# Optimization experiments

Hardware: AMD Instinct MI355X
Metric: run time of the kernel (lower is better)

The kernel has to match this reference:

```python
import jax, jax.numpy as jnp
import numpy as np

K = 16  # kNN neighbors (global k in the original source)
# channel progression of the 6 DynamicEdgeConv layers
DIMS = [3, 32, 128, 256, 64, 32, 16]


def _knn_idx(x, k):
    # x: [B, N, D] -> indices of k nearest neighbors (incl. self), [B, N, k]
    sq = jnp.sum(x * x, axis=-1)                                   # [B, N]
    d = sq[:, :, None] + sq[:, None, :] - 2.0 * jnp.einsum('bnd,bmd->bnm', x, x)
    _, idx = jax.lax.top_k(-d, k)                                  # smallest distances
    return idx


def _edge_conv(x, W1, b1, W2, b2, k):
    # DynamicEdgeConv with mean aggregation: message = MLP([x_i, x_j - x_i])
    idx = _knn_idx(x, k)                                           # [B, N, k]
    xj = jax.vmap(lambda xb, ib: xb[ib])(x, idx)                   # [B, N, k, D]
    xi = jnp.broadcast_to(x[:, :, None, :], xj.shape)
    e = jnp.concatenate([xi, xj - xi], axis=-1)                    # [B, N, k, 2D]
    h = jax.nn.relu(e @ W1 + b1)
    h = jax.nn.relu(h @ W2 + b2)
    return jnp.mean(h, axis=2)                                     # [B, N, d_out]


def setup_inputs() -> dict:
    key = jax.random.key(0)
    ks = jax.random.split(key, 32)
    inp = {'x': jax.random.normal(ks[0], (8, 2048, 3), dtype=jnp.float32)}
    for l in range(6):
        din, dout = DIMS[l], DIMS[l + 1]
        s1 = 1.0 / np.sqrt(2 * din)
        s2 = 1.0 / np.sqrt(2 * dout)
        inp[f'W1_{l}'] = jax.random.normal(ks[1 + 4 * l], (2 * din, 2 * dout), dtype=jnp.float32) * s1
        inp[f'b1_{l}'] = jnp.zeros((2 * dout,), dtype=jnp.float32)
        inp[f'W2_{l}'] = jax.random.normal(ks[2 + 4 * l], (2 * dout, dout), dtype=jnp.float32) * s2
        inp[f'b2_{l}'] = jnp.zeros((dout,), dtype=jnp.float32)
    inp['Wf'] = jax.random.normal(ks[30], (16, 2), dtype=jnp.float32) * 0.25
    inp['bf'] = jnp.zeros((2,), dtype=jnp.float32)
    return inp


def reference(x, W1_0, b1_0, W2_0, b2_0, W1_1, b1_1, W2_1, b2_1,
              W1_2, b1_2, W2_2, b2_2, W1_3, b1_3, W2_3, b2_3,
              W1_4, b1_4, W2_4, b2_4, W1_5, b1_5, W2_5, b2_5, Wf, bf):
    params = [(W1_0, b1_0, W2_0, b2_0), (W1_1, b1_1, W2_1, b2_1),
              (W1_2, b1_2, W2_2, b2_2), (W1_3, b1_3, W2_3, b2_3),
              (W1_4, b1_4, W2_4, b2_4), (W1_5, b1_5, W2_5, b2_5)]
    for (W1, b1, W2, b2) in params:
        x = _edge_conv(x, W1, b1, W2, b2, K)
        x = jax.nn.relu(x)  # extra ReLU from forward (dropout is eval-mode identity)
    pooled = jnp.mean(x, axis=1)        # global_mean_pool over nodes -> [B, 16]
    return pooled @ Wf + bf             # [B, 2]
```

## Files before the change

### kernel.cpp

```cpp
#include <hip/hip_runtime.h>
#include <math.h>

#define NPTS 2048
#define NB 8
#define BN 16384
#define KNN 16

typedef _Float16 half4 __attribute__((ext_vector_type(4)));
typedef _Float16 half8 __attribute__((ext_vector_type(8)));
typedef float floatx16 __attribute__((ext_vector_type(16)));

__global__ __launch_bounds__(256) void sqprep_kernel(const float* __restrict__ X,
                                                     float* __restrict__ SQ,
                                                     const float* __restrict__ W1,
                                                     const float* __restrict__ b1,
                                                     float* __restrict__ Wcat,
                                                     float* __restrict__ bcat,
                                                     int din, int d2,
                                                     const float* __restrict__ W2,
                                                     _Float16* __restrict__ W2H,
                                                     _Float16* __restrict__ W2L,
                                                     int dout, int pb) {
    const int bid = blockIdx.x;
    if (bid < BN / 256) {
        int g = bid * 256 + threadIdx.x;
        const float* row = X + (size_t)g * din;
        float s = 0.f;
        for (int d = 0; d < din; ++d) s = fmaf(row[d], row[d], s);
        SQ[g] = s;
    } else if (bid < BN / 256 + pb) {
        int n4 = 2 * d2;
        int total = din * n4;
        int i = (bid - BN / 256) * 256 + threadIdx.x;
        if (i < total) {
            int d = i / n4, c = i - d * n4;
            float v;
            if (c < d2) v = W1[d * d2 + c] - W1[(din + d) * d2 + c];
            else        v = W1[(din + d) * d2 + (c - d2)];
            Wcat[i] = v;
        }
        if (i < n4) bcat[i] = (i < d2) ? b1[i] : 0.f;
    } else {
        int i = (bid - BN / 256 - pb) * 256 + threadIdx.x;
        if (i < d2 * dout) {
            int k = i / dout, c = i - k * dout;
            float wv = W2[i];
            _Float16 hv = (_Float16)wv;
            float rv = wv - (float)hv;
            W2H[(size_t)c * d2 + k] = hv;
            W2L[(size_t)c * d2 + k] = (_Float16)rv;
        }
    }
}

template <int DIN>
__global__ __launch_bounds__(256) void gram_kernel(const float* __restrict__ X,
                                                   const float* __restrict__ SQ,
                                                   float* __restrict__ DT) {
    __shared__ float As[32][132];
    __shared__ float Bs[32][132];
    const int t = threadIdx.x;
    const int tx = t & 15, ty = t >> 4;
    int bid = blockIdx.x;
    int bi = 0;
    while (bid >= 16 - bi) { bid -= 16 - bi; ++bi; }
    const int bj = bi + bid;
    const int i0 = bi * 128;
    const int j0 = bj * 128;
    const int z = blockIdx.z;
    const float* Xb = X + (size_t)z * NPTS * DIN;
    const float* SQb = SQ + (size_t)z * NPTS;
    float* DTb = DT + (size_t)z * NPTS * NPTS;

    const int e = t & 127;

    float acc[8][8];
    #pragma unroll
    for (int i = 0; i < 8; ++i)
        #pragma unroll
        for (int j = 0; j < 8; ++j) acc[i][j] = 0.f;

    if constexpr (DIN % 32 == 0) {
        const int rh = (t >> 7) * 16;
        const float* Ar = Xb + (size_t)(i0 + e) * DIN;
        const float* Br = Xb + (size_t)(j0 + e) * DIN;
        for (int k0 = 0; k0 < DIN; k0 += 32) {
            #pragma unroll
            for (int h = 0; h < 4; ++h) {
                float4 a = *(const float4*)(Ar + k0 + rh + h * 4);
                float4 b = *(const float4*)(Br + k0 + rh + h * 4);
                As[rh + h * 4 + 0][e] = a.x; As[rh + h * 4 + 1][e] = a.y;
                As[rh + h * 4 + 2][e] = a.z; As[rh + h * 4 + 3][e] = a.w;
                Bs[rh + h * 4 + 0][e] = b.x; Bs[rh + h * 4 + 1][e] = b.y;
                Bs[rh + h * 4 + 2][e] = b.z; Bs[rh + h * 4 + 3][e] = b.w;
            }
            __syncthreads();
            #pragma unroll
            for (int r = 0; r < 32; ++r) {
                float4 a0 = *(const float4*)&As[r][ty * 4];
                float4 a1 = *(const float4*)&As[r][64 + ty * 4];
                float4 b0 = *(const float4*)&Bs[r][tx * 4];
                float4 b1 = *(const float4*)&Bs[r][64 + tx * 4];
                float av[8] = {a0.x, a0.y, a0.z, a0.w, a1.x, a1.y, a1.z, a1.w};
                float bv[8] = {b0.x, b0.y, b0.z, b0.w, b1.x, b1.y, b1.z, b1.w};
                #pragma unroll
                for (int i = 0; i < 8; ++i)
                    #pragma unroll
                    for (int j = 0; j < 8; ++j)
                        acc[i][j] = fmaf(av[i], bv[j], acc[i][j]);
            }
            __syncthreads();
        }
    } else {
        const int rh = (t >> 7) * 8;
        #pragma unroll
        for (int i = 0; i < 8; ++i) {
            int k = rh + i;
            As[rh + i][e] = (k < DIN) ? Xb[(size_t)(i0 + e) * DIN + k] : 0.f;
            Bs[rh + i][e] = (k < DIN) ? Xb[(size_t)(j0 + e) * DIN + k] : 0.f;
        }
        __syncthreads();
        #pragma unroll
        for (int r = 0; r < 16; ++r) {
            float4 a0 = *(const float4*)&As[r][ty * 4];
            float4 a1 = *(const float4*)&As[r][64 + ty * 4];
            float4 b0 = *(const float4*)&Bs[r][tx * 4];
            float4 b1 = *(const float4*)&Bs[r][64 + tx * 4];
            float av[8] = {a0.x, a0.y, a0.z, a0.w, a1.x, a1.y, a1.z, a1.w};
            float bv[8] = {b0.x, b0.y, b0.z, b0.w, b1.x, b1.y, b1.z, b1.w};
            #pragma unroll
            for (int i = 0; i < 8; ++i)
                #pragma unroll
                for (int j = 0; j < 8; ++j)
                    acc[i][j] = fmaf(av[i], bv[j], acc[i][j]);
        }
        __syncthreads();
    }

    float sqi[8], sqj[8];
    #pragma unroll
    for (int i = 0; i < 8; ++i) {
        int ro = (i < 4) ? (ty * 4 + i) : (64 + ty * 4 + (i - 4));
        sqi[i] = SQb[i0 + ro];
    }
    #pragma unroll
    for (int j = 0; j < 8; ++j) {
        int co = (j < 4) ? (tx * 4 + j) : (64 + tx * 4 + (j - 4));
        sqj[j] = SQb[j0 + co];
    }
    #pragma unroll
    for (int i = 0; i < 8; ++i) {
        int ro = (i < 4) ? (ty * 4 + i) : (64 + ty * 4 + (i - 4));
        float* out = DTb + (size_t)(i0 + ro) * NPTS + j0;
        float4 o0, o1;
        o0.x = (sqi[i] + sqj[0]) - 2.f * acc[i][0];
        o0.y = (sqi[i] + sqj[1]) - 2.f * acc[i][1];
        o0.z = (sqi[i] + sqj[2]) - 2.f * acc[i][2];
        o0.w = (sqi[i] + sqj[3]) - 2.f * acc[i][3];
        o1.x = (sqi[i] + sqj[4]) - 2.f * acc[i][4];
        o1.y = (sqi[i] + sqj[5]) - 2.f * acc[i][5];
        o1.z = (sqi[i] + sqj[6]) - 2.f * acc[i][6];
        o1.w = (sqi[i] + sqj[7]) - 2.f * acc[i][7];
        *(float4*)(out + tx * 4) = o0;
        *(float4*)(out + 64 + tx * 4) = o1;
    }
    if (bi != bj) {
        #pragma unroll
        for (int j = 0; j < 8; ++j) {
            int co = (j < 4) ? (tx * 4 + j) : (64 + tx * 4 + (j - 4));
            float* out = DTb + (size_t)(j0 + co) * NPTS + i0;
            float4 o0, o1;
            o0.x = (sqi[0] + sqj[j]) - 2.f * acc[0][j];
            o0.y = (sqi[1] + sqj[j]) - 2.f * acc[1][j];
            o0.z = (sqi[2] + sqj[j]) - 2.f * acc[2][j];
            o0.w = (sqi[3] + sqj[j]) - 2.f * acc[3][j];
            o1.x = (sqi[4] + sqj[j]) - 2.f * acc[4][j];
            o1.y = (sqi[5] + sqj[j]) - 2.f * acc[5][j];
            o1.z = (sqi[6] + sqj[j]) - 2.f * acc[6][j];
            o1.w = (sqi[7] + sqj[j]) - 2.f * acc[7][j];
            *(float4*)(out + ty * 4) = o0;
            *(float4*)(out + 64 + ty * 4) = o1;
        }
    }
}

__global__ __launch_bounds__(256) void knn_select_kernel(const float* __restrict__ DT,
                                                         int* __restrict__ IDX, int qoff) {
    const int t = threadIdx.x;
    const int w = t >> 6, lane = t & 63;
    const int q = blockIdx.x * 4 + w;
    const float* dq = DT + (size_t)q * NPTS;
    const int l4 = lane << 2;

    float vals[32];
    #pragma unroll
    for (int s = 0; s < 8; ++s) {
        float4 v = *(const float4*)(dq + s * 256 + l4);
        vals[s * 4 + 0] = v.x; vals[s * 4 + 1] = v.y;
        vals[s * 4 + 2] = v.z; vals[s * 4 + 3] = v.w;
    }
    unsigned rm = 0;
    float best = INFINITY; int bslot = 32;
    #pragma unroll
    for (int sl = 0; sl < 32; ++sl)
        if (vals[sl] < best) { best = vals[sl]; bslot = sl; }

    for (int rep = 0; rep < KNN; ++rep) {
        int bj = (bslot < 32) ? ((bslot >> 2) * 256 + l4 + (bslot & 3)) : NPTS;
        float gb = best; int gj = bj;
        #pragma unroll
        for (int off = 1; off < 64; off <<= 1) {
            float ov = __shfl_xor(gb, off);
            int oj = __shfl_xor(gj, off);
            if (ov < gb || (ov == gb && oj < gj)) { gb = ov; gj = oj; }
        }
        if (lane == 0) IDX[(size_t)(qoff + q) * KNN + rep] = gj;
        if (((gj >> 2) & 63) == lane) {
            int slot = ((gj >> 8) << 2) | (gj & 3);
            rm |= (1u << slot);
            best = INFINITY; bslot = 32;
            #pragma unroll
            for (int sl = 0; sl < 32; ++sl)
                if (!(rm & (1u << sl)) && vals[sl] < best) { best = vals[sl]; bslot = sl; }
        }
    }
}

template <int KK, int NN>
__global__ __launch_bounds__(256) void gemm_big_kernel(const float* __restrict__ A,
                                                       const float* __restrict__ B,
                                                       const float* __restrict__ bias,
                                                       float* __restrict__ C) {
    __shared__ float As[32][132];
    __shared__ float Bs[32][132];
    const int t = threadIdx.x;
    const int tx = t & 15, ty = t >> 4;
    const int m0 = blockIdx.x * 128;
    const int c0 = blockIdx.y * 128;

    float acc[8][8];
    #pragma unroll
    for (int i = 0; i < 8; ++i)
        #pragma unroll
        for (int j = 0; j < 8; ++j) acc[i][j] = 0.f;

    const int e = t & 127;
    const int rh = (t >> 7) * 16;
    const float* Ar = A + (size_t)(m0 + e) * KK + rh;
    const int br = t & 31;
    const int bc = (t >> 5) * 16;
    const float* Wbase = B + (size_t)br * NN + c0 + bc;

    for (int k0 = 0; k0 < KK; k0 += 32) {
        #pragma unroll
        for (int h = 0; h < 4; ++h) {
            float4 a = *(const float4*)(Ar + k0 + h * 4);
            As[rh + h * 4 + 0][e] = a.x; As[rh + h * 4 + 1][e] = a.y;
            As[rh + h * 4 + 2][e] = a.z; As[rh + h * 4 + 3][e] = a.w;
            *(float4*)&Bs[br][bc + h * 4] = *(const float4*)(Wbase + (size_t)k0 * NN + h * 4);
        }
        __syncthreads();
        #pragma unroll
        for (int r = 0; r < 32; ++r) {
            float4 a0 = *(const float4*)&As[r][ty * 4];
            float4 a1 = *(const float4*)&As[r][64 + ty * 4];
            float4 b0 = *(const float4*)&Bs[r][tx * 4];
            float4 b1 = *(const float4*)&Bs[r][64 + tx * 4];
            float av[8] = {a0.x, a0.y, a0.z, a0.w, a1.x, a1.y, a1.z, a1.w};
            float bv[8] = {b0.x, b0.y, b0.z, b0.w, b1.x, b1.y, b1.z, b1.w};
            #pragma unroll
            for (int i = 0; i < 8; ++i)
                #pragma unroll
                for (int j = 0; j < 8; ++j)
                    acc[i][j] = fmaf(av[i], bv[j], acc[i][j]);
        }
        __syncthreads();
    }

    float bvv[8];
    #pragma unroll
    for (int j = 0; j < 8; ++j) {
        int co = (j < 4) ? (tx * 4 + j) : (64 + tx * 4 + (j - 4));
        bvv[j] = bias[c0 + co];
    }
    #pragma unroll
    for (int i = 0; i < 8; ++i) {
        int ro = (i < 4) ? (ty * 4 + i) : (64 + ty * 4 + (i - 4));
        float* out = C + (size_t)(m0 + ro) * NN + c0;
        float4 o0, o1;
        o0.x = acc[i][0] + bvv[0]; o0.y = acc[i][1] + bvv[1];
        o0.z = acc[i][2] + bvv[2]; o0.w = acc[i][3] + bvv[3];
        o1.x = acc[i][4] + bvv[4]; o1.y = acc[i][5] + bvv[5];
        o1.z = acc[i][6] + bvv[6]; o1.w = acc[i][7] + bvv[7];
        *(float4*)(out + tx * 4) = o0;
        *(float4*)(out + 64 + tx * 4) = o1;
    }
}

template <int KK, int NN>
__global__ __launch_bounds__(256) void gemm_pq_kernel(const float* __restrict__ A,
                                                      const float* __restrict__ B,
                                                      const float* __restrict__ bias,
                                                      float* __restrict__ C) {
    __shared__ float As[16][68];
    __shared__ float Bs[16][64];
    const int t = threadIdx.x;
    const int tx = t & 15, ty = t >> 4;
    const int m0 = blockIdx.x * 64;
    const int c0 = blockIdx.y * 64;
    float acc[4][4];
    #pragma unroll
    for (int i = 0; i < 4; ++i)
        #pragma unroll
        for (int j = 0; j < 4; ++j) acc[i][j] = 0.f;

    constexpr int KCH = (KK + 15) / 16;
    for (int kc = 0; kc < KCH; ++kc) {
        const int k0 = kc * 16;
        {
            int m = t & 63;
            int r4 = (t >> 6) * 4;
            if constexpr (KK % 16 == 0) {
                float4 v = *(const float4*)(A + (size_t)(m0 + m) * KK + k0 + r4);
                As[r4 + 0][m] = v.x; As[r4 + 1][m] = v.y;
                As[r4 + 2][m] = v.z; As[r4 + 3][m] = v.w;
            } else {
                #pragma unroll
                for (int i = 0; i < 4; ++i) {
                    int r = r4 + i;
                    As[r][m] = (k0 + r < KK) ? A[(size_t)(m0 + m) * KK + k0 + r] : 0.f;
                }
            }
        }
        {
            int r = t >> 4;
            int c = (t & 15) * 4;
            float4 v = make_float4(0.f, 0.f, 0.f, 0.f);
            if (k0 + r < KK) v = *(const float4*)(B + (size_t)(k0 + r) * NN + c0 + c);
            *(float4*)&Bs[r][c] = v;
        }
        __syncthreads();
        #pragma unroll
        for (int r = 0; r < 16; ++r) {
            float4 a4 = *(const float4*)&As[r][ty * 4];
            float4 b4 = *(const float4*)&Bs[r][tx * 4];
            float av[4] = {a4.x, a4.y, a4.z, a4.w};
            float bv[4] = {b4.x, b4.y, b4.z, b4.w};
            #pragma unroll
            for (int i = 0; i < 4; ++i)
                #pragma unroll
                for (int j = 0; j < 4; ++j)
                    acc[i][j] = fmaf(av[i], bv[j], acc[i][j]);
        }
        __syncthreads();
    }
    float4 bv4 = *(const float4*)(bias + c0 + tx * 4);
    float bv[4] = {bv4.x, bv4.y, bv4.z, bv4.w};
    #pragma unroll
    for (int i = 0; i < 4; ++i) {
        float4 o;
        o.x = acc[i][0] + bv[0];
        o.y = acc[i][1] + bv[1];
        o.z = acc[i][2] + bv[2];
        o.w = acc[i][3] + bv[3];
        *(float4*)(C + (size_t)(m0 + ty * 4 + i) * NN + c0 + tx * 4) = o;
    }
}

template <int D2, int DOUT>
__global__ __launch_bounds__(256) void edge_kernel(const float* __restrict__ PQ,
                                                   const int* __restrict__ IDX,
                                                   const float* __restrict__ W2,
                                                   const float* __restrict__ b2,
                                                   float* __restrict__ Xn) {
    constexpr int N4 = 2 * D2;
    __shared__ float As[16][68];
    __shared__ float Bs[16][64];
    __shared__ int gjs[64];
    const int t = threadIdx.x;
    const int tx = t & 15, ty = t >> 4;
    const int nb = blockIdx.x * 4;
    const int c0 = blockIdx.y * 64;

    if (t < 64) {
        int node = nb + (t >> 4);
        int bstart = (node / NPTS) * NPTS;
        gjs[t] = bstart + IDX[(size_t)node * KNN + (t & 15)];
    }
    __syncthreads();

    float acc[4][4];
    #pragma unroll
    for (int i = 0; i < 4; ++i)
        #pragma unroll
        for (int j = 0; j < 4; ++j) acc[i][j] = 0.f;

    const int e = t & 63;
    const int r4 = (t >> 6) * 4;
    const int gi = nb + (e >> 4);

    for (int k0 = 0; k0 < D2; k0 += 16) {
        {
            int gj = gjs[e];
            float4 p = *(const float4*)(PQ + (size_t)gi * N4 + k0 + r4);
            float4 q = *(const float4*)(PQ + (size_t)gj * N4 + D2 + k0 + r4);
            As[r4 + 0][e] = fmaxf(p.x + q.x, 0.f);
            As[r4 + 1][e] = fmaxf(p.y + q.y, 0.f);
            As[r4 + 2][e] = fmaxf(p.z + q.z, 0.f);
            As[r4 + 3][e] = fmaxf(p.w + q.w, 0.f);
        }
        {
            int r = t >> 4;
            int c = (t & 15) * 4;
            float4 v = make_float4(0.f, 0.f, 0.f, 0.f);
            if (c0 + c < DOUT) v = *(const float4*)(W2 + (size_t)(k0 + r) * DOUT + c0 + c);
            *(float4*)&Bs[r][c] = v;
        }
        __syncthreads();
        #pragma unroll
        for (int r = 0; r < 16; ++r) {
            float4 a4 = *(const float4*)&As[r][ty * 4];
            float4 b4 = *(const float4*)&Bs[r][tx * 4];
            float av[4] = {a4.x, a4.y, a4.z, a4.w};
            float bv[4] = {b4.x, b4.y, b4.z, b4.w};
            #pragma unroll
            for (int i = 0; i < 4; ++i)
                #pragma unroll
                for (int j = 0; j < 4; ++j)
                    acc[i][j] = fmaf(av[i], bv[j], acc[i][j]);
        }
        __syncthreads();
    }

    float bv[4];
    #pragma unroll
    for (int j = 0; j < 4; ++j) {
        int c = c0 + tx * 4 + j;
        bv[j] = (c < DOUT) ? b2[c] : 0.f;
    }
    float s[4];
    #pragma unroll
    for (int j = 0; j < 4; ++j) {
        float ss = 0.f;
        #pragma unroll
        for (int i = 0; i < 4; ++i) ss += fmaxf(acc[i][j] + bv[j], 0.f);
        s[j] = ss;
    }
    #pragma unroll
    for (int j = 0; j < 4; ++j) Bs[ty][tx * 4 + j] = s[j];
    __syncthreads();
    if ((ty & 3) == 0) {
        int node = nb + (ty >> 2);
        #pragma unroll
        for (int j = 0; j < 4; ++j) {
            int c = c0 + tx * 4 + j;
            if (c < DOUT) {
                int cc = tx * 4 + j;
                float tot = Bs[ty][cc] + Bs[ty + 1][cc] + Bs[ty + 2][cc] + Bs[ty + 3][cc];
                Xn[(size_t)node * DOUT + c] = tot * (1.f / 16.f);
            }
        }
    }
}

template <int D2, int DOUT>
__global__ __launch_bounds__(256) void edge_mid_kernel(const float* __restrict__ PQ,
                                                       const int* __restrict__ IDX,
                                                       const float* __restrict__ W2,
                                                       const float* __restrict__ b2,
                                                       float* __restrict__ Xn) {
    constexpr int N4 = 2 * D2;
    __shared__ float As[32][132];
    __shared__ float Bs[32][68];
    __shared__ int gjs[128];
    const int t = threadIdx.x;
    const int tx = t & 15, ty = t >> 4;
    const int nb8 = blockIdx.x * 8;

    if (t < 128) {
        int node = nb8 + (t >> 4);
        int bstart = (node / NPTS) * NPTS;
        gjs[t] = bstart + IDX[(size_t)node * KNN + (t & 15)];
    }
    __syncthreads();

    float acc[8][4];
    #pragma unroll
    for (int i = 0; i < 8; ++i)
        #pragma unroll
        for (int j = 0; j < 4; ++j) acc[i][j] = 0.f;

    const int e = t & 127;
    const int rh = (t >> 7) * 16;
    const int gi = nb8 + (e >> 4);
    const int gj = gjs[e];
    const float* Prow = PQ + (size_t)gi * N4;
    const float* Qrow = PQ + (size_t)gj * N4 + D2;
    const int br = t & 31;
    const int bc = (t >> 5) * 8;
    const float* Wbase = W2 + (size_t)br * DOUT + bc;

    for (int k0 = 0; k0 < D2; k0 += 32) {
        #pragma unroll
        for (int h = 0; h < 4; ++h) {
            float4 p = *(const float4*)(Prow + k0 + rh + h * 4);
            float4 q = *(const float4*)(Qrow + k0 + rh + h * 4);
            As[rh + h * 4 + 0][e] = fmaxf(p.x + q.x, 0.f);
            As[rh + h * 4 + 1][e] = fmaxf(p.y + q.y, 0.f);
            As[rh + h * 4 + 2][e] = fmaxf(p.z + q.z, 0.f);
            As[rh + h * 4 + 3][e] = fmaxf(p.w + q.w, 0.f);
        }
        {
            const float* wp = Wbase + (size_t)k0 * DOUT;
            *(float4*)&Bs[br][bc] = *(const float4*)(wp);
            *(float4*)&Bs[br][bc + 4] = *(const float4*)(wp + 4);
        }
        __syncthreads();
        #pragma unroll
        for (int r = 0; r < 32; ++r) {
            float4 a0 = *(const float4*)&As[r][ty * 4];
            float4 a1 = *(const float4*)&As[r][64 + ty * 4];
            float4 b0 = *(const float4*)&Bs[r][tx * 4];
            float av[8] = {a0.x, a0.y, a0.z, a0.w, a1.x, a1.y, a1.z, a1.w};
            float bv[4] = {b0.x, b0.y, b0.z, b0.w};
            #pragma unroll
            for (int i = 0; i < 8; ++i)
                #pragma unroll
                for (int j = 0; j < 4; ++j)
                    acc[i][j] = fmaf(av[i], bv[j], acc[i][j]);
        }
        __syncthreads();
    }

    #pragma unroll
    for (int j = 0; j < 4; ++j) {
        int cl = tx * 4 + j;
        float bb = b2[cl];
        float s0 = 0.f, s1 = 0.f;
        #pragma unroll
        for (int i = 0; i < 4; ++i) {
            s0 += fmaxf(acc[i][j] + bb, 0.f);
            s1 += fmaxf(acc[4 + i][j] + bb, 0.f);
        }
        As[ty][cl] = s0;
        Bs[ty][cl] = s1;
    }
    __syncthreads();
    if (t < 128) {
        int node = t >> 4;
        int colb = (t & 15) * 4;
        int tg = (node & 3) * 4;
        float v0, v1, v2, v3;
        if (node < 4) {
            v0 = As[tg + 0][colb + 0] + As[tg + 1][colb + 0] + As[tg + 2][colb + 0] + As[tg + 3][colb + 0];
            v1 = As[tg + 0][colb + 1] + As[tg + 1][colb + 1] + As[tg + 2][colb + 1] + As[tg + 3][colb + 1];
            v2 = As[tg + 0][colb + 2] + As[tg + 1][colb + 2] + As[tg + 2][colb + 2] + As[tg + 3][colb + 2];
            v3 = As[tg + 0][colb + 3] + As[tg + 1][colb + 3] + As[tg + 2][colb + 3] + As[tg + 3][colb + 3];
        } else {
            v0 = Bs[tg + 0][colb + 0] + Bs[tg + 1][colb + 0] + Bs[tg + 2][colb + 0] + Bs[tg + 3][colb + 0];
            v1 = Bs[tg + 0][colb + 1] + Bs[tg + 1][colb + 1] + Bs[tg + 2][colb + 1] + Bs[tg + 3][colb + 1];
            v2 = Bs[tg + 0][colb + 2] + Bs[tg + 1][colb + 2] + Bs[tg + 2][colb + 2] + Bs[tg + 3][colb + 2];
            v3 = Bs[tg + 0][colb + 3] + Bs[tg + 1][colb + 3] + Bs[tg + 2][colb + 3] + Bs[tg + 3][colb + 3];
        }
        float4 o;
        o.x = v0 * (1.f / 16.f); o.y = v1 * (1.f / 16.f);
        o.z = v2 * (1.f / 16.f); o.w = v3 * (1.f / 16.f);
        *(float4*)(Xn + (size_t)(nb8 + node) * DOUT + colb) = o;
    }
}

template <int D2, int DOUT>
__global__ __launch_bounds__(256) void edge_big_mfma_kernel(const float* __restrict__ PQ,
                                                            const int* __restrict__ IDX,
                                                            const _Float16* __restrict__ W2H,
                                                            const _Float16* __restrict__ W2L,
                                                            const float* __restrict__ b2,
                                                            float* __restrict__ Xn) {
    constexpr int N4 = 2 * D2;
    __shared__ _Float16 Ah[128][40];
    __shared__ _Float16 Al[128][40];
    __shared__ _Float16 Bh[128][40];
    __shared__ _Float16 Bl[128][40];
    __shared__ int gjs[128];
    const int t = threadIdx.x;
    const int nb8 = blockIdx.x * 8;
    const int c0 = blockIdx.y * 128;

    if (t < 128) {
        int node = nb8 + (t >> 4);
        int bstart = (node / NPTS) * NPTS;
        gjs[t] = bstart + IDX[(size_t)node * KNN + (t & 15)];
    }
    __syncthreads();

    const int e = t & 127;
    const int rh = (t >> 7) * 16;
    const int gi = nb8 + (e >> 4);
    const int gj = gjs[e];
    const float* Prow = PQ + (size_t)gi * N4;
    const float* Qrow = PQ + (size_t)gj * N4 + D2;
    const _Float16* WHrow = W2H + (size_t)(c0 + e) * D2;
    const _Float16* WLrow = W2L + (size_t)(c0 + e) * D2;

    const int w = t >> 6;
    const int lane = t & 63;
    const int wr = (w >> 1) * 64;
    const int wc = (w & 1) * 64;
    const int lr = lane & 31;
    const int lk = (lane >> 5) * 8;
    const int hsel = lane >> 5;

    floatx16 acc[2][2];
    #pragma unroll
    for (int i = 0; i < 2; ++i)
        #pragma unroll
        for (int j = 0; j < 2; ++j)
            #pragma unroll
            for (int r = 0; r < 16; ++r) acc[i][j][r] = 0.f;

    for (int k0 = 0; k0 < D2; k0 += 32) {
        #pragma unroll
        for (int h = 0; h < 4; ++h) {
            float4 p = *(const float4*)(Prow + k0 + rh + h * 4);
            float4 q = *(const float4*)(Qrow + k0 + rh + h * 4);
            float a0 = fmaxf(p.x + q.x, 0.f);
            float a1 = fmaxf(p.y + q.y, 0.f);
            float a2 = fmaxf(p.z + q.z, 0.f);
            float a3 = fmaxf(p.w + q.w, 0.f);
            _Float16 h0 = (_Float16)a0, h1 = (_Float16)a1, h2 = (_Float16)a2, h3 = (_Float16)a3;
            half4 hv, lv;
            hv.x = h0; hv.y = h1; hv.z = h2; hv.w = h3;
            lv.x = (_Float16)(a0 - (float)h0);
            lv.y = (_Float16)(a1 - (float)h1);
            lv.z = (_Float16)(a2 - (float)h2);
            lv.w = (_Float16)(a3 - (float)h3);
            *(half4*)&Ah[e][rh + h * 4] = hv;
            *(half4*)&Al[e][rh + h * 4] = lv;
        }
        *(half8*)&Bh[e][rh]     = *(const half8*)(WHrow + k0 + rh);
        *(half8*)&Bh[e][rh + 8] = *(const half8*)(WHrow + k0 + rh + 8);
        *(half8*)&Bl[e][rh]     = *(const half8*)(WLrow + k0 + rh);
        *(half8*)&Bl[e][rh + 8] = *(const half8*)(WLrow + k0 + rh + 8);
        __syncthreads();
        #pragma unroll
        for (int ks = 0; ks < 2; ++ks) {
            half8 af[2], alf[2], bf[2], blf[2];
            #pragma unroll
            for (int i = 0; i < 2; ++i) {
                af[i]  = *(const half8*)&Ah[wr + i * 32 + lr][ks * 16 + lk];
                alf[i] = *(const half8*)&Al[wr + i * 32 + lr][ks * 16 + lk];
                bf[i]  = *(const half8*)&Bh[wc + i * 32 + lr][ks * 16 + lk];
                blf[i] = *(const half8*)&Bl[wc + i * 32 + lr][ks * 16 + lk];
            }
            #pragma unroll
            for (int i = 0; i < 2; ++i)
                #pragma unroll
                for (int j = 0; j < 2; ++j) {
                    acc[i][j] = __builtin_amdgcn_mfma_f32_32x32x16_f16(af[i],  bf[j],  acc[i][j], 0, 0, 0);
                    acc[i][j] = __builtin_amdgcn_mfma_f32_32x32x16_f16(af[i],  blf[j], acc[i][j], 0, 0, 0);
                    acc[i][j] = __builtin_amdgcn_mfma_f32_32x32x16_f16(alf[i], bf[j],  acc[i][j], 0, 0, 0);
                }
        }
        __syncthreads();
    }

    float bb[2];
    bb[0] = b2[c0 + wc + lr];
    bb[1] = b2[c0 + wc + 32 + lr];
    #pragma unroll
    for (int i = 0; i < 2; ++i) {
        int node0 = nb8 + ((wr + i * 32) >> 4);
        #pragma unroll
        for (int j = 0; j < 2; ++j) {
            float sA = 0.f, sB = 0.f;
            #pragma unroll
            for (int r = 0; r < 8; ++r)  sA += fmaxf(acc[i][j][r] + bb[j], 0.f);
            #pragma unroll
            for (int r = 8; r < 16; ++r) sB += fmaxf(acc[i][j][r] + bb[j], 0.f);
            sA += __shfl_xor(sA, 32);
            sB += __shfl_xor(sB, 32);
            if (hsel == 0) {
                int col = c0 + wc + j * 32 + lr;
                Xn[(size_t)node0 * DOUT + col] = sA * (1.f / 16.f);
                Xn[(size_t)(node0 + 1) * DOUT + col] = sB * (1.f / 16.f);
            }
        }
    }
}

__global__ __launch_bounds__(256) void final_kernel(const float* __restrict__ X,
                                                    const float* __restrict__ Wf,
                                                    const float* __restrict__ bfin,
                                                    float* __restrict__ out) {
    __shared__ float red[16][17];
    __shared__ float pool[16];
    const int b = blockIdx.x;
    const int t = threadIdx.x;
    const int c = t & 15, rg = t >> 4;
    float s = 0.f;
    for (int n = rg; n < NPTS; n += 16) s += X[(size_t)(b * NPTS + n) * 16 + c];
    red[rg][c] = s;
    __syncthreads();
    if (t < 16) {
        float tot = 0.f;
        #pragma unroll
        for (int i = 0; i < 16; ++i) tot += red[i][t];
        pool[t] = tot * (1.f / NPTS);
    }
    __syncthreads();
    if (t < 2) {
        float a = bfin[t];
        #pragma unroll
        for (int cc = 0; cc < 16; ++cc) a = fmaf(pool[cc], Wf[cc * 2 + t], a);
        out[b * 2 + t] = a;
    }
}

template <int DIN, int DOUT>
static void run_layer(const float* Xin, float* Xout, float* PQ, float* SQ, int* IDX,
                      float* WCAT, float* BCAT, _Float16* W2H, _Float16* W2L,
                      const float* W1, const float* b1, const float* W2, const float* b2,
                      hipStream_t stream) {
    constexpr int D2 = 2 * DOUT;
    constexpr int N4 = 2 * D2;
    constexpr int prep_blocks = (DIN * N4 + 255) / 256;
    constexpr int w2_blocks = (DOUT >= 128) ? ((D2 * DOUT + 255) / 256) : 0;
    sqprep_kernel<<<BN / 256 + prep_blocks + w2_blocks, 256, 0, stream>>>(
        Xin, SQ, W1, b1, WCAT, BCAT, DIN, D2, W2, W2H, W2L,
        (DOUT >= 128) ? DOUT : 0, prep_blocks);
    for (int h = 0; h < 2; ++h) {
        dim3 gg(136, 1, 4);
        gram_kernel<DIN><<<gg, 256, 0, stream>>>(Xin + (size_t)h * 4 * NPTS * DIN,
                                                 SQ + (size_t)h * 4 * NPTS, PQ);
        knn_select_kernel<<<2048, 256, 0, stream>>>(PQ, IDX, h * 8192);
    }
    if constexpr (N4 % 128 == 0 && DIN % 32 == 0) {
        dim3 g1(BN / 128, N4 / 128);
        gemm_big_kernel<DIN, N4><<<g1, 256, 0, stream>>>(Xin, WCAT, BCAT, PQ);
    } else {
        dim3 g1(BN / 64, N4 / 64);
        gemm_pq_kernel<DIN, N4><<<g1, 256, 0, stream>>>(Xin, WCAT, BCAT, PQ);
    }
    if constexpr (DOUT >= 128) {
        dim3 g2(BN / 8, DOUT / 128);
        edge_big_mfma_kernel<D2, DOUT><<<g2, 256, 0, stream>>>(PQ, IDX, W2H, W2L, b2, Xout);
    } else if constexpr (DOUT == 64) {
        dim3 g2(BN / 8, 1);
        edge_mid_kernel<D2, DOUT><<<g2, 256, 0, stream>>>(PQ, IDX, W2, b2, Xout);
    } else {
        dim3 g2(BN / 4, (DOUT + 63) / 64);
        edge_kernel<D2, DOUT><<<g2, 256, 0, stream>>>(PQ, IDX, W2, b2, Xout);
    }
}

extern "C" void kernel_launch(void* const* d_in, const int* in_sizes, int n_in,
                              void* d_out, int out_size, void* d_ws, size_t ws_size,
                              hipStream_t stream) {
    (void)in_sizes; (void)n_in; (void)out_size; (void)ws_size;
    const float* x = (const float*)d_in[0];
    const float* W1a[6]; const float* b1a[6]; const float* W2a[6]; const float* b2a[6];
    for (int l = 0; l < 6; ++l) {
        W1a[l] = (const float*)d_in[1 + 4 * l];
        b1a[l] = (const float*)d_in[2 + 4 * l];
        W2a[l] = (const float*)d_in[3 + 4 * l];
        b2a[l] = (const float*)d_in[4 + 4 * l];
    }
    const float* Wf = (const float*)d_in[25];
    const float* bfin = (const float*)d_in[26];

    float* ws = (float*)d_ws;
    float* X0   = ws;
    float* X1   = X0 + (size_t)BN * 256;
    float* PQ   = X1 + (size_t)BN * 256;
    float* SQ   = PQ + (size_t)BN * 1024;
    int*   IDX  = (int*)(SQ + BN);
    float* WCAT = (float*)(IDX + (size_t)BN * KNN);
    float* BCAT = WCAT + 131072;
    _Float16* W2H = (_Float16*)(BCAT + 1024);
    _Float16* W2L = W2H + 131072;

    run_layer<3,   32>(x,  X0, PQ, SQ, IDX, WCAT, BCAT, W2H, W2L, W1a[0], b1a[0], W2a[0], b2a[0], stream);
    run_layer<32, 128>(X0, X1, PQ, SQ, IDX, WCAT, BCAT, W2H, W2L, W1a[1], b1a[1], W2a[1], b2a[1], stream);
    run_layer<128,256>(X1, X0, PQ, SQ, IDX, WCAT, BCAT, W2H, W2L, W1a[2], b1a[2], W2a[2], b2a[2], stream);
    run_layer<256, 64>(X0, X1, PQ, SQ, IDX, WCAT, BCAT, W2H, W2L, W1a[3], b1a[3], W2a[3], b2a[3], stream);
    run_layer<64,  32>(X1, X0, PQ, SQ, IDX, WCAT, BCAT, W2H, W2L, W1a[4], b1a[4], W2a[4], b2a[4], stream);
    run_layer<32,  16>(X0, X1, PQ, SQ, IDX, WCAT, BCAT, W2H, W2L, W1a[5], b1a[5], W2a[5], b2a[5], stream);
    final_kernel<<<NB, 256, 0, stream>>>(X1, Wf, bfin, (float*)d_out);
}
```

Before: 1.947 ms.

## Port DOUT=64 edge kernel to split-fp16 MFMA and prefetch PQ in big kernel

Replaces the scalar FP32 edge_mid_kernel used for the DOUT=64 layer with an MFMA kernel. It uses split hi/lo fp16 operands to keep near-FP32 accuracy, and the W2 hi/lo conversion prep is extended to the DOUT=64 case. Both the new mid kernel and the big MFMA kernel now software-prefetch the next K-slice of P/Q rows into registers after the barrier and load W2 before the LDS writes. The second __syncthreads is replaced by a raw s_barrier, and B fragments are hoisted so they are reused across the row tiles. This aims to cut FP32 ALU time and hide global load latency, at the cost of higher register pressure and three MFMAs per product.

```diff
diff --git a/kernel.cpp b/kernel.cpp
--- a/kernel.cpp
+++ b/kernel.cpp
@@ -464,112 +464,6 @@
 }
 
 template <int D2, int DOUT>
-__global__ __launch_bounds__(256) void edge_mid_kernel(const float* __restrict__ PQ,
-                                                       const int* __restrict__ IDX,
-                                                       const float* __restrict__ W2,
-                                                       const float* __restrict__ b2,
-                                                       float* __restrict__ Xn) {
-    constexpr int N4 = 2 * D2;
-    __shared__ float As[32][132];
-    __shared__ float Bs[32][68];
-    __shared__ int gjs[128];
-    const int t = threadIdx.x;
-    const int tx = t & 15, ty = t >> 4;
-    const int nb8 = blockIdx.x * 8;
-
-    if (t < 128) {
-        int node = nb8 + (t >> 4);
-        int bstart = (node / NPTS) * NPTS;
-        gjs[t] = bstart + IDX[(size_t)node * KNN + (t & 15)];
-    }
-    __syncthreads();
-
-    float acc[8][4];
-    #pragma unroll
-    for (int i = 0; i < 8; ++i)
-        #pragma unroll
-        for (int j = 0; j < 4; ++j) acc[i][j] = 0.f;
-
-    const int e = t & 127;
-    const int rh = (t >> 7) * 16;
-    const int gi = nb8 + (e >> 4);
-    const int gj = gjs[e];
-    const float* Prow = PQ + (size_t)gi * N4;
-    const float* Qrow = PQ + (size_t)gj * N4 + D2;
-    const int br = t & 31;
-    const int bc = (t >> 5) * 8;
-    const float* Wbase = W2 + (size_t)br * DOUT + bc;
-
-    for (int k0 = 0; k0 < D2; k0 += 32) {
-        #pragma unroll
-        for (int h = 0; h < 4; ++h) {
-            float4 p = *(const float4*)(Prow + k0 + rh + h * 4);
-            float4 q = *(const float4*)(Qrow + k0 + rh + h * 4);
-            As[rh + h * 4 + 0][e] = fmaxf(p.x + q.x, 0.f);
-            As[rh + h * 4 + 1][e] = fmaxf(p.y + q.y, 0.f);
-            As[rh + h * 4 + 2][e] = fmaxf(p.z + q.z, 0.f);
-            As[rh + h * 4 + 3][e] = fmaxf(p.w + q.w, 0.f);
-        }
-        {
-            const float* wp = Wbase + (size_t)k0 * DOUT;
-            *(float4*)&Bs[br][bc] = *(const float4*)(wp);
-            *(float4*)&Bs[br][bc + 4] = *(const float4*)(wp + 4);
-        }
-        __syncthreads();
-        #pragma unroll
-        for (int r = 0; r < 32; ++r) {
-            float4 a0 = *(const float4*)&As[r][ty * 4];
-            float4 a1 = *(const float4*)&As[r][64 + ty * 4];
-            float4 b0 = *(const float4*)&Bs[r][tx * 4];
-            float av[8] = {a0.x, a0.y, a0.z, a0.w, a1.x, a1.y, a1.z, a1.w};
-            float bv[4] = {b0.x, b0.y, b0.z, b0.w};
-            #pragma unroll
-            for (int i = 0; i < 8; ++i)
-                #pragma unroll
-                for (int j = 0; j < 4; ++j)
-                    acc[i][j] = fmaf(av[i], bv[j], acc[i][j]);
-        }
-        __syncthreads();
-    }
-
-    #pragma unroll
-    for (int j = 0; j < 4; ++j) {
-        int cl = tx * 4 + j;
-        float bb = b2[cl];
-        float s0 = 0.f, s1 = 0.f;
-        #pragma unroll
-        for (int i = 0; i < 4; ++i) {
-            s0 += fmaxf(acc[i][j] + bb, 0.f);
-            s1 += fmaxf(acc[4 + i][j] + bb, 0.f);
-        }
-        As[ty][cl] = s0;
-        Bs[ty][cl] = s1;
-    }
-    __syncthreads();
-    if (t < 128) {
-        int node = t >> 4;
-        int colb = (t & 15) * 4;
-        int tg = (node & 3) * 4;
-        float v0, v1, v2, v3;
-        if (node < 4) {
-            v0 = As[tg + 0][colb + 0] + As[tg + 1][colb + 0] + As[tg + 2][colb + 0] + As[tg + 3][colb + 0];
-            v1 = As[tg + 0][colb + 1] + As[tg + 1][colb + 1] + As[tg + 2][colb + 1] + As[tg + 3][colb + 1];
-            v2 = As[tg + 0][colb + 2] + As[tg + 1][colb + 2] + As[tg + 2][colb + 2] + As[tg + 3][colb + 2];
-            v3 = As[tg + 0][colb + 3] + As[tg + 1][colb + 3] + As[tg + 2][colb + 3] + As[tg + 3][colb + 3];
-        } else {
-            v0 = Bs[tg + 0][colb + 0] + Bs[tg + 1][colb + 0] + Bs[tg + 2][colb + 0] + Bs[tg + 3][colb + 0];
-            v1 = Bs[tg + 0][colb + 1] + Bs[tg + 1][colb + 1] + Bs[tg + 2][colb + 1] + Bs[tg + 3][colb + 1];
-            v2 = Bs[tg + 0][colb + 2] + Bs[tg + 1][colb + 2] + Bs[tg + 2][colb + 2] + Bs[tg + 3][colb + 2];
-            v3 = Bs[tg + 0][colb + 3] + Bs[tg + 1][colb + 3] + Bs[tg + 2][colb + 3] + Bs[tg + 3][colb + 3];
-        }
-        float4 o;
-        o.x = v0 * (1.f / 16.f); o.y = v1 * (1.f / 16.f);
-        o.z = v2 * (1.f / 16.f); o.w = v3 * (1.f / 16.f);
-        *(float4*)(Xn + (size_t)(nb8 + node) * DOUT + colb) = o;
-    }
-}
-
-template <int D2, int DOUT>
 __global__ __launch_bounds__(256) void edge_big_mfma_kernel(const float* __restrict__ PQ,
                                                             const int* __restrict__ IDX,
                                                             const _Float16* __restrict__ W2H,
@@ -618,15 +512,24 @@
             #pragma unroll
             for (int r = 0; r < 16; ++r) acc[i][j][r] = 0.f;
 
+    float4 pp[4], qq[4];
+    #pragma unroll
+    for (int h = 0; h < 4; ++h) {
+        pp[h] = *(const float4*)(Prow + rh + h * 4);
+        qq[h] = *(const float4*)(Qrow + rh + h * 4);
+    }
+
     for (int k0 = 0; k0 < D2; k0 += 32) {
+        half8 wh0 = *(const half8*)(WHrow + k0 + rh);
+        half8 wh1 = *(const half8*)(WHrow + k0 + rh + 8);
+        half8 wl0 = *(const half8*)(WLrow + k0 + rh);
+        half8 wl1 = *(const half8*)(WLrow + k0 + rh + 8);
         #pragma unroll
         for (int h = 0; h < 4; ++h) {
-            float4 p = *(const float4*)(Prow + k0 + rh + h * 4);
-            float4 q = *(const float4*)(Qrow + k0 + rh + h * 4);
-            float a0 = fmaxf(p.x + q.x, 0.f);
-            float a1 = fmaxf(p.y + q.y, 0.f);
-            float a2 = fmaxf(p.z + q.z, 0.f);
-            float a3 = fmaxf(p.w + q.w, 0.f);
+            float a0 = fmaxf(pp[h].x + qq[h].x, 0.f);
+            float a1 = fmaxf(pp[h].y + qq[h].y, 0.f);
+            float a2 = fmaxf(pp[h].z + qq[h].z, 0.f);
+            float a3 = fmaxf(pp[h].w + qq[h].w, 0.f);
             _Float16 h0 = (_Float16)a0, h1 = (_Float16)a1, h2 = (_Float16)a2, h3 = (_Float16)a3;
             half4 hv, lv;
             hv.x = h0; hv.y = h1; hv.z = h2; hv.w = h3;
@@ -637,31 +540,40 @@
             *(half4*)&Ah[e][rh + h * 4] = hv;
             *(half4*)&Al[e][rh + h * 4] = lv;
         }
-        *(half8*)&Bh[e][rh]     = *(const half8*)(WHrow + k0 + rh);
-        *(half8*)&Bh[e][rh + 8] = *(const half8*)(WHrow + k0 + rh + 8);
-        *(half8*)&Bl[e][rh]     = *(const half8*)(WLrow + k0 + rh);
-        *(half8*)&Bl[e][rh + 8] = *(const half8*)(WLrow + k0 + rh + 8);
-        __syncthreads();
+        *(half8*)&Bh[e][rh]     = wh0;
+        *(half8*)&Bh[e][rh + 8] = wh1;
+        *(half8*)&Bl[e][rh]     = wl0;
+        *(half8*)&Bl[e][rh + 8] = wl1;
+        __syncthreads();
+        if (k0 + 32 < D2) {
+            #pragma unroll
+            for (int h = 0; h < 4; ++h) {
+                pp[h] = *(const float4*)(Prow + k0 + 32 + rh + h * 4);
+                qq[h] = *(const float4*)(Qrow + k0 + 32 + rh + h * 4);
+            }
+        }
         #pragma unroll
         for (int ks = 0; ks < 2; ++ks) {
-            half8 af[2], alf[2], bf[2], blf[2];
+            const int kb = ks * 16 + lk;
+            half8 bf0  = *(const half8*)&Bh[wc + lr][kb];
+            half8 blf0 = *(const half8*)&Bl[wc + lr][kb];
+            half8 bf1  = *(const half8*)&Bh[wc + 32 + lr][kb];
+            half8 blf1 = *(const half8*)&Bl[wc + 32 + lr][kb];
             #pragma unroll
             for (int i = 0; i < 2; ++i) {
-                af[i]  = *(const half8*)&Ah[wr + i * 32 + lr][ks * 16 + lk];
-                alf[i] = *(const half8*)&Al[wr + i * 32 + lr][ks * 16 + lk];
-                bf[i]  = *(const half8*)&Bh[wc + i * 32 + lr][ks * 16 + lk];
-                blf[i] = *(const half8*)&Bl[wc + i * 32 + lr][ks * 16 + lk];
+                half8 af  = *(const half8*)&Ah[wr + i * 32 + lr][kb];
+                half8 alf = *(const half8*)&Al[wr + i * 32 + lr][kb];
+                acc[i][0] = __builtin_amdgcn_mfma_f32_32x32x16_f16(af,  bf0,  acc[i][0], 0, 0, 0);
+                acc[i][0] = __builtin_amdgcn_mfma_f32_32x32x16_f16(af,  blf0, acc[i][0], 0, 0, 0);
+                acc[i][0] = __builtin_amdgcn_mfma_f32_32x32x16_f16(alf, bf0,  acc[i][0], 0, 0, 0);
+                acc[i][1] = __builtin_amdgcn_mfma_f32_32x32x16_f16(af,  bf1,  acc[i][1], 0, 0, 0);
+                acc[i][1] = __builtin_amdgcn_mfma_f32_32x32x16_f16(af,  blf1, acc[i][1], 0, 0, 0);
+                acc[i][1] = __builtin_amdgcn_mfma_f32_32x32x16_f16(alf, bf1,  acc[i][1], 0, 0, 0);
             }
-            #pragma unroll
-            for (int i = 0; i < 2; ++i)
-                #pragma unroll
-                for (int j = 0; j < 2; ++j) {
-                    acc[i][j] = __builtin_amdgcn_mfma_f32_32x32x16_f16(af[i],  bf[j],  acc[i][j], 0, 0, 0);
-                    acc[i][j] = __builtin_amdgcn_mfma_f32_32x32x16_f16(af[i],  blf[j], acc[i][j], 0, 0, 0);
-                    acc[i][j] = __builtin_amdgcn_mfma_f32_32x32x16_f16(alf[i], bf[j],  acc[i][j], 0, 0, 0);
-                }
-        }
-        __syncthreads();
+        }
+        asm volatile("" ::: "memory");
+        __builtin_amdgcn_s_barrier();
+        asm volatile("" ::: "memory");
     }
 
     float bb[2];
@@ -684,6 +596,128 @@
                 Xn[(size_t)node0 * DOUT + col] = sA * (1.f / 16.f);
                 Xn[(size_t)(node0 + 1) * DOUT + col] = sB * (1.f / 16.f);
             }
+        }
+    }
+}
+
+template <int D2, int DOUT>
+__global__ __launch_bounds__(256) void edge_mid_mfma_kernel(const float* __restrict__ PQ,
+                                                            const int* __restrict__ IDX,
+                                                            const _Float16* __restrict__ W2H,
+                                                            const _Float16* __restrict__ W2L,
+                                                            const float* __restrict__ b2,
+                                                            float* __restrict__ Xn) {
+    constexpr int N4 = 2 * D2;
+    __shared__ _Float16 Ah[128][40];
+    __shared__ _Float16 Al[128][40];
+    __shared__ _Float16 Bh[64][40];
+    __shared__ _Float16 Bl[64][40];
+    __shared__ int gjs[128];
+    const int t = threadIdx.x;
+    const int nb8 = blockIdx.x * 8;
+
+    if (t < 128) {
+        int node = nb8 + (t >> 4);
+        int bstart = (node / NPTS) * NPTS;
+        gjs[t] = bstart + IDX[(size_t)node * KNN + (t & 15)];
+    }
+    __syncthreads();
+
+    const int e = t & 127;
+    const int rh = (t >> 7) * 16;
+    const int gi = nb8 + (e >> 4);
+    const int gj = gjs[e];
+    const float* Prow = PQ + (size_t)gi * N4;
+    const float* Qrow = PQ + (size_t)gj * N4 + D2;
+    const int wrB = t & 63;
+    const int wkB = (t >> 6) * 8;
+    const _Float16* WHrow = W2H + (size_t)wrB * D2 + wkB;
+    const _Float16* WLrow = W2L + (size_t)wrB * D2 + wkB;
+
+    const int w = t >> 6;
+    const int lane = t & 63;
+    const int wr = (w >> 1) * 64;
+    const int wc = (w & 1) * 32;
+    const int lr = lane & 31;
+    const int lk = (lane >> 5) * 8;
+    const int hsel = lane >> 5;
+
+    floatx16 acc[2];
+    #pragma unroll
+    for (int i = 0; i < 2; ++i)
+        #pragma unroll
+        for (int r = 0; r < 16; ++r) acc[i][r] = 0.f;
+
+    float4 pp[4], qq[4];
+    #pragma unroll
+    for (int h = 0; h < 4; ++h) {
+        pp[h] = *(const float4*)(Prow + rh + h * 4);
+        qq[h] = *(const float4*)(Qrow + rh + h * 4);
+    }
+
+    for (int k0 = 0; k0 < D2; k0 += 32) {
+        half8 wh0 = *(const half8*)(WHrow + k0);
+        half8 wl0 = *(const half8*)(WLrow + k0);
+        #pragma unroll
+        for (int h = 0; h < 4; ++h) {
+            float a0 = fmaxf(pp[h].x + qq[h].x, 0.f);
+            float a1 = fmaxf(pp[h].y + qq[h].y, 0.f);
+            float a2 = fmaxf(pp[h].z + qq[h].z, 0.f);
+            float a3 = fmaxf(pp[h].w + qq[h].w, 0.f);
+            _Float16 h0 = (_Float16)a0, h1 = (_Float16)a1, h2 = (_Float16)a2, h3 = (_Float16)a3;
+            half4 hv, lv;
+            hv.x = h0; hv.y = h1; hv.z = h2; hv.w = h3;
+            lv.x = (_Float16)(a0 - (float)h0);
+            lv.y = (_Float16)(a1 - (float)h1);
+            lv.z = (_Float16)(a2 - (float)h2);
+            lv.w = (_Float16)(a3 - (float)h3);
+            *(half4*)&Ah[e][rh + h * 4] = hv;
+            *(half4*)&Al[e][rh + h * 4] = lv;
+        }
+        *(half8*)&Bh[wrB][wkB] = wh0;
+        *(half8*)&Bl[wrB][wkB] = wl0;
+        __syncthreads();
+        if (k0 + 32 < D2) {
+            #pragma unroll
+            for (int h = 0; h < 4; ++h) {
+                pp[h] = *(const float4*)(Prow + k0 + 32 + rh + h * 4);
+                qq[h] = *(const float4*)(Qrow + k0 + 32 + rh + h * 4);
+            }
+        }
+        #pragma unroll
+        for (int ks = 0; ks < 2; ++ks) {
+            const int kb = ks * 16 + lk;
+            half8 bf0  = *(const half8*)&Bh[wc + lr][kb];
+            half8 blf0 = *(const half8*)&Bl[wc + lr][kb];
+            #pragma unroll
+            for (int i = 0; i < 2; ++i) {
+                half8 af  = *(const half8*)&Ah[wr + i * 32 + lr][kb];
+                half8 alf = *(const half8*)&Al[wr + i * 32 + lr][kb];
+                acc[i] = __builtin_amdgcn_mfma_f32_32x32x16_f16(af,  bf0,  acc[i], 0, 0, 0);
+                acc[i] = __builtin_amdgcn_mfma_f32_32x32x16_f16(af,  blf0, acc[i], 0, 0, 0);
+                acc[i] = __builtin_amdgcn_mfma_f32_32x32x16_f16(alf, bf0,  acc[i], 0, 0, 0);
+            }
+        }
+        asm volatile("" ::: "memory");
+        __builtin_amdgcn_s_barrier();
+        asm volatile("" ::: "memory");
+    }
+
+    float bb = b2[wc + lr];
+    #pragma unroll
+    for (int i = 0; i < 2; ++i) {
+        int node0 = nb8 + ((wr + i * 32) >> 4);
+        float sA = 0.f, sB = 0.f;
+        #pragma unroll
+        for (int r = 0; r < 8; ++r)  sA += fmaxf(acc[i][r] + bb, 0.f);
+        #pragma unroll
+        for (int r = 8; r < 16; ++r) sB += fmaxf(acc[i][r] + bb, 0.f);
+        sA += __shfl_xor(sA, 32);
+        sB += __shfl_xor(sB, 32);
+        if (hsel == 0) {
+            int col = wc + lr;
+            Xn[(size_t)node0 * DOUT + col] = sA * (1.f / 16.f);
+            Xn[(size_t)(node0 + 1) * DOUT + col] = sB * (1.f / 16.f);
         }
     }
 }
@@ -724,10 +758,10 @@
     constexpr int D2 = 2 * DOUT;
     constexpr int N4 = 2 * D2;
     constexpr int prep_blocks = (DIN * N4 + 255) / 256;
-    constexpr int w2_blocks = (DOUT >= 128) ? ((D2 * DOUT + 255) / 256) : 0;
+    constexpr int w2_blocks = (DOUT >= 64) ? ((D2 * DOUT + 255) / 256) : 0;
     sqprep_kernel<<<BN / 256 + prep_blocks + w2_blocks, 256, 0, stream>>>(
         Xin, SQ, W1, b1, WCAT, BCAT, DIN, D2, W2, W2H, W2L,
-        (DOUT >= 128) ? DOUT : 0, prep_blocks);
+        (DOUT >= 64) ? DOUT : 0, prep_blocks);
     for (int h = 0; h < 2; ++h) {
         dim3 gg(136, 1, 4);
         gram_kernel<DIN><<<gg, 256, 0, stream>>>(Xin + (size_t)h * 4 * NPTS * DIN,
@@ -746,7 +780,7 @@
         edge_big_mfma_kernel<D2, DOUT><<<g2, 256, 0, stream>>>(PQ, IDX, W2H, W2L, b2, Xout);
     } else if constexpr (DOUT == 64) {
         dim3 g2(BN / 8, 1);
-        edge_mid_kernel<D2, DOUT><<<g2, 256, 0, stream>>>(PQ, IDX, W2, b2, Xout);
+        edge_mid_mfma_kernel<D2, DOUT><<<g2, 256, 0, stream>>>(PQ, IDX, W2H, W2L, b2, Xout);
     } else {
         dim3 g2(BN / 4, (DOUT + 63) / 64);
         edge_kernel<D2, DOUT><<<g2, 256, 0, stream>>>(PQ, IDX, W2, b2, Xout);
```

After: 1.852 ms. 4.8% less time.
